# Performance work log

Measured on AMD Instinct MI355X. Metric: run time of the kernel, lower is better.

Reference implementation:

```python
import jax, jax.numpy as jnp
import numpy as np

IC = 8      # inter_channels = in_channels // 2
K = 5       # top-k
EPS = 1e-5  # BatchNorm eps


def _conv(x, w, b, stride, pad):
    y = jax.lax.conv_general_dilated(
        x, w, (stride, stride), [(pad, pad), (pad, pad)],
        dimension_numbers=('NCHW', 'OIHW', 'NCHW'))
    return y + b[None, :, None, None]


def _maxpool2(x):
    return jax.lax.reduce_window(x, -jnp.inf, jax.lax.max,
                                 (1, 1, 2, 2), (1, 1, 2, 2), 'VALID')


def _up2(x):
    return jnp.repeat(jnp.repeat(x, 2, axis=2), 2, axis=3)


def setup_inputs() -> dict:
    key = jax.random.key(0)
    ks = jax.random.split(key, 12)
    C = 16
    x_ms = jax.random.normal(ks[0], (1, C, 96, 96), jnp.float32)
    hp_pan = jax.random.normal(ks[1], (1, C, 192, 192), jnp.float32)
    x_pan = jax.random.normal(ks[2], (1, C, 192, 192), jnp.float32)
    s = 0.05
    return {
        'x_ms': x_ms, 'hp_pan': hp_pan, 'x_pan': x_pan,
        'g_w': jax.random.normal(ks[3], (IC, C, 1, 1), jnp.float32) * s,
        'g_b': jax.random.normal(ks[4], (IC,), jnp.float32) * s,
        'theta_w': jax.random.normal(ks[5], (IC, C, 3, 3), jnp.float32) * s,
        'theta_b': jax.random.normal(ks[6], (IC,), jnp.float32) * s,
        'phi_w': jax.random.normal(ks[7], (IC, C, 3, 3), jnp.float32) * s,
        'phi_b': jax.random.normal(ks[8], (IC,), jnp.float32) * s,
        'W_w': jax.random.normal(ks[9], (C, IC, 1, 1), jnp.float32) * s,
        'W_b': jax.random.normal(ks[10], (C,), jnp.float32) * s,
        'bn_gamma': jax.random.normal(ks[11], (C,), jnp.float32) * s + 1.0,
        'bn_beta': jnp.zeros((C,), jnp.float32),
    }


def reference(x_ms, hp_pan, x_pan, g_w, g_b, theta_w, theta_b,
              phi_w, phi_b, W_w, W_b, bn_gamma, bn_beta):
    B, _, H, W = x_ms.shape
    # g: 1x1 conv + maxpool2 on hp_pan -> (B, M, IC)
    g_x = _maxpool2(_conv(hp_pan, g_w, g_b, 1, 0))
    g_x = g_x.reshape(B, IC, -1).transpose(0, 2, 1)
    # theta: 3x3 s2 conv + up2 on x_ms -> (B, N, IC), N = H*W
    th = _up2(_conv(x_ms, theta_w, theta_b, 2, 1))
    th = th.reshape(B, IC, -1).transpose(0, 2, 1)
    # phi: 3x3 s2 conv + maxpool2 + up2 on x_pan -> (B, IC, M)
    ph = _up2(_maxpool2(_conv(x_pan, phi_w, phi_b, 2, 1)))
    ph = ph.reshape(B, IC, -1)
    # dense similarity (B, N, M)
    f = jnp.einsum('bnc,bcm->bnm', th, ph)
    scores, idx = jax.lax.top_k(f, K)            # (B, N, K)
    scores = jax.nn.softmax(scores, axis=-1)
    # weighted matmul with V restricted to top-k columns (same math as
    # scatter-into-zeros followed by dense matmul, without the dense zeros)
    bi = jnp.arange(B)[:, None, None]
    g_sel = g_x[bi, idx]                          # (B, N, K, IC)
    y = jnp.einsum('bnk,bnkc->bnc', scores, g_sel)
    y = y.transpose(0, 2, 1).reshape(B, IC, H, W)
    wy = _conv(y, W_w, W_b, 1, 0)
    # BatchNorm2d (training-mode batch statistics)
    mean = wy.mean(axis=(0, 2, 3), keepdims=True)
    var = wy.var(axis=(0, 2, 3), keepdims=True)
    z = (wy - mean) * jax.lax.rsqrt(var + EPS)
    z = z * bn_gamma[None, :, None, None] + bn_beta[None, :, None, None]
    return (z, x_pan)
```

## Files before the change

### kernel.cpp

```cpp
#include <hip/hip_runtime.h>

#define IC 8
#define NC 2304
#define NF 9216
#define Z_ELEMS 147456
#define XPAN_ELEMS 589824

typedef unsigned int uint_t;

__global__ __launch_bounds__(256) void k1_prep(
    const float* __restrict__ xms,
    const float* __restrict__ hppan,
    const float* __restrict__ xpan,
    const float* __restrict__ gw, const float* __restrict__ gb,
    const float* __restrict__ thw, const float* __restrict__ thb,
    const float* __restrict__ phw, const float* __restrict__ phb,
    float* __restrict__ theta_c,
    float* __restrict__ phi_c,
    float* __restrict__ gmat)
{
    const int b = blockIdx.x;
    const int tid = threadIdx.x;

    if (b < 18) {
        int idx = b * 256 + tid;
        int pix = idx >> 1, half = idx & 1;
        int r = pix / 48, c = pix % 48;
        int ir0 = 2 * r - 1, ic0 = 2 * c - 1;
        bool rok = (r > 0), cok = (c > 0);
        float acc[8];
        #pragma unroll
        for (int co = 0; co < 8; ++co) acc[co] = 0.0f;
        int ci0 = half * 8;
        #pragma unroll 4
        for (int ci8 = 0; ci8 < 8; ++ci8) {
            int ci = ci0 + ci8;
            const float* base = xms + ci * 9216;
            float xv[9];
            #pragma unroll
            for (int dr = 0; dr < 3; ++dr) {
                #pragma unroll
                for (int dc = 0; dc < 3; ++dc) {
                    bool ok = (dr > 0 || rok) && (dc > 0 || cok);
                    int off = (ir0 + dr) * 96 + (ic0 + dc);
                    float v = base[ok ? off : 0];
                    xv[dr * 3 + dc] = ok ? v : 0.0f;
                }
            }
            #pragma unroll
            for (int tap = 0; tap < 9; ++tap) {
                #pragma unroll
                for (int co = 0; co < 8; ++co)
                    acc[co] += thw[co * 144 + ci * 9 + tap] * xv[tap];
            }
        }
        #pragma unroll
        for (int co = 0; co < 8; ++co) {
            float v = acc[co] + __shfl_xor(acc[co], 1);
            if (half == 0) theta_c[pix * 8 + co] = v + thb[co];
        }
    } else if (b < 90) {
        int idx = (b - 18) * 256 + tid;
        int half = idx & 1, sp = (idx >> 1) & 3, cp = idx >> 3;
        int rc = cp / 48, cc = cp % 48;
        int r96 = 2 * rc + (sp >> 1), c96 = 2 * cc + (sp & 1);
        int ir0 = 2 * r96 - 1, ic0 = 2 * c96 - 1;
        bool rok = (r96 > 0), cok = (c96 > 0);
        float acc[8];
        #pragma unroll
        for (int co = 0; co < 8; ++co) acc[co] = 0.0f;
        int ci0 = half * 8;
        #pragma unroll 4
        for (int ci8 = 0; ci8 < 8; ++ci8) {
            int ci = ci0 + ci8;
            const float* base = xpan + ci * 36864;
            float xv[9];
            #pragma unroll
            for (int dr = 0; dr < 3; ++dr) {
                #pragma unroll
                for (int dc = 0; dc < 3; ++dc) {
                    bool ok = (dr > 0 || rok) && (dc > 0 || cok);
                    int off = (ir0 + dr) * 192 + (ic0 + dc);
                    float v = base[ok ? off : 0];
                    xv[dr * 3 + dc] = ok ? v : 0.0f;
                }
            }
            #pragma unroll
            for (int tap = 0; tap < 9; ++tap) {
                #pragma unroll
                for (int co = 0; co < 8; ++co)
                    acc[co] += phw[co * 144 + ci * 9 + tap] * xv[tap];
            }
        }
        #pragma unroll
        for (int co = 0; co < 8; ++co) {
            float v = acc[co] + __shfl_xor(acc[co], 1);
            v = fmaxf(v, __shfl_xor(v, 2));
            v = fmaxf(v, __shfl_xor(v, 4));
            if ((idx & 7) == 0) phi_c[cp * 8 + co] = v + phb[co];
        }
    } else {
        int idx = (b - 90) * 256 + tid;
        int op = idx >> 2, sp = idx & 3;
        int r = 2 * (op / 96) + (sp >> 1), c = 2 * (op % 96) + (sp & 1);
        const float* bp = hppan + r * 192 + c;
        float acc[8];
        #pragma unroll
        for (int co = 0; co < 8; ++co) acc[co] = 0.0f;
        #pragma unroll
        for (int ci = 0; ci < 16; ++ci) {
            float xv = bp[ci * 36864];
            #pragma unroll
            for (int co = 0; co < 8; ++co)
                acc[co] += gw[co * 16 + ci] * xv;
        }
        #pragma unroll
        for (int co = 0; co < 8; ++co) {
            float v = acc[co];
            v = fmaxf(v, __shfl_xor(v, 1));
            v = fmaxf(v, __shfl_xor(v, 2));
            if (sp == 0) gmat[op * 8 + co] = v + gb[co];
        }
    }
}

__global__ __launch_bounds__(256) void k2_attn(
    const float* __restrict__ theta_c, const float* __restrict__ phi_c,
    const float* __restrict__ gmat, float* __restrict__ y_c)
{
    const int tid = threadIdx.x;
    const int wv = tid >> 6, lane = tid & 63;
    const int nc0 = blockIdx.x * 4;

    float th[4][8];
    #pragma unroll
    for (int r = 0; r < 4; ++r)
        #pragma unroll
        for (int j = 0; j < 8; ++j)
            th[r][j] = theta_c[(nc0 + r) * 8 + j];

    float v1[4], v2[4];
    int i1[4], i2[4];
    #pragma unroll
    for (int r = 0; r < 4; ++r) {
        v1[r] = -INFINITY; v2[r] = -INFINITY;
        i1[r] = 0x7fffffff; i2[r] = 0x7fffffff;
    }

    #pragma unroll
    for (int it = 0; it < 9; ++it) {
        int mc = lane + ((it * 4 + wv) << 6);
        const float4* p = (const float4*)(phi_c + mc * 8);
        float4 a = p[0], bq = p[1];
        #pragma unroll
        for (int r = 0; r < 4; ++r) {
            float v = th[r][0] * a.x + th[r][1] * a.y + th[r][2] * a.z + th[r][3] * a.w
                    + th[r][4] * bq.x + th[r][5] * bq.y + th[r][6] * bq.z + th[r][7] * bq.w;
            if (v > v1[r])      { v2[r] = v1[r]; i2[r] = i1[r]; v1[r] = v; i1[r] = mc; }
            else if (v > v2[r]) { v2[r] = v; i2[r] = mc; }
        }
    }

    #pragma unroll
    for (int r = 0; r < 4; ++r) {
        #pragma unroll
        for (int off = 1; off < 64; off <<= 1) {
            float ov1 = __shfl_xor(v1[r], off);
            int   oi1 = __shfl_xor(i1[r], off);
            float ov2 = __shfl_xor(v2[r], off);
            int   oi2 = __shfl_xor(i2[r], off);
            bool afirst = (v1[r] > ov1) || (v1[r] == ov1 && i1[r] < oi1);
            if (afirst) {
                bool t = (v2[r] > ov1) || (v2[r] == ov1 && i2[r] < oi1);
                v2[r] = t ? v2[r] : ov1; i2[r] = t ? i2[r] : oi1;
            } else {
                bool t = (ov2 > v1[r]) || (ov2 == v1[r] && oi2 < i1[r]);
                float nv2 = t ? ov2 : v1[r]; int ni2 = t ? oi2 : i1[r];
                v1[r] = ov1; i1[r] = oi1; v2[r] = nv2; i2[r] = ni2;
            }
        }
    }

    __shared__ float cv1[4][4], cv2[4][4];
    __shared__ int   ci1[4][4], ci2[4][4];
    if (lane == 0) {
        #pragma unroll
        for (int r = 0; r < 4; ++r) {
            cv1[wv][r] = v1[r]; ci1[wv][r] = i1[r];
            cv2[wv][r] = v2[r]; ci2[wv][r] = i2[r];
        }
    }
    __syncthreads();

    if (tid < 32) {
        int r = tid >> 3, ch = tid & 7;
        float m1 = -INFINITY, m2 = -INFINITY;
        int j1 = 0x7fffffff, j2 = 0x7fffffff;
        #pragma unroll
        for (int w = 0; w < 4; ++w) {
            #pragma unroll
            for (int s = 0; s < 2; ++s) {
                float v = s ? cv2[w][r] : cv1[w][r];
                int   i = s ? ci2[w][r] : ci1[w][r];
                bool b1 = (v > m1) || (v == m1 && i < j1);
                bool b2 = (v > m2) || (v == m2 && i < j2);
                if (b1)      { m2 = m1; j2 = j1; m1 = v; j1 = i; }
                else if (b2) { m2 = v; j2 = i; }
            }
        }
        int rc1 = j1 / 48, cc1 = j1 % 48;
        int m00 = (2 * rc1) * 96 + 2 * cc1;
        int rc2 = j2 / 48, cc2 = j2 % 48;
        int mm2 = (2 * rc2) * 96 + 2 * cc2;
        float e = __expf(m2 - m1);
        float inv = 1.0f / (4.0f + e);
        float gs = gmat[m00 * 8 + ch] + gmat[(m00 + 1) * 8 + ch]
                 + gmat[(m00 + 96) * 8 + ch] + gmat[(m00 + 97) * 8 + ch];
        y_c[(nc0 + r) * 8 + ch] = inv * gs + (e * inv) * gmat[mm2 * 8 + ch];
    }
}

__global__ __launch_bounds__(256) void k3_out(
    const float* __restrict__ y_c,
    const float* __restrict__ Ww, const float* __restrict__ Wb,
    const float* __restrict__ gamma, const float* __restrict__ beta,
    const float* __restrict__ xpan,
    float* __restrict__ zout, float* __restrict__ xpan_out)
{
    const int b = blockIdx.x;
    const int tid = threadIdx.x;

    if (b >= 16) {
        int i = (b - 16) * 256 + tid;
        ((uint4*)xpan_out)[i] = ((const uint4*)xpan)[i];
        return;
    }

    const int co = b;
    float w[8];
    #pragma unroll
    for (int j = 0; j < 8; ++j) w[j] = Ww[co * 8 + j];
    const float bias = Wb[co];

    float wy[9];
    float s = 0.f, s2 = 0.f;
    #pragma unroll
    for (int j = 0; j < 9; ++j) {
        int mc = tid + j * 256;
        const float4* p = (const float4*)(y_c + mc * 8);
        float4 a = p[0], bq = p[1];
        float v = bias + w[0] * a.x + w[1] * a.y + w[2] * a.z + w[3] * a.w
                       + w[4] * bq.x + w[5] * bq.y + w[6] * bq.z + w[7] * bq.w;
        wy[j] = v; s += v; s2 += v * v;
    }
    #pragma unroll
    for (int off = 32; off; off >>= 1) {
        s  += __shfl_down(s, off);
        s2 += __shfl_down(s2, off);
    }
    __shared__ float ps[4], ps2[4];
    __shared__ float sc_s, sh_s;
    int wv = tid >> 6, lane = tid & 63;
    if (lane == 0) { ps[wv] = s; ps2[wv] = s2; }
    __syncthreads();
    if (tid == 0) {
        float S  = ps[0] + ps[1] + ps[2] + ps[3];
        float S2 = ps2[0] + ps2[1] + ps2[2] + ps2[3];
        float mean = S * (1.0f / 2304.0f);
        float var  = S2 * (1.0f / 2304.0f) - mean * mean;
        float rsig = 1.0f / sqrtf(var + 1e-5f);
        float gm = gamma[co], be = beta[co];
        sc_s = gm * rsig;
        sh_s = be - mean * gm * rsig;
    }
    __syncthreads();
    float sc = sc_s, sh = sh_s;
    #pragma unroll
    for (int j = 0; j < 9; ++j) {
        int mc = tid + j * 256;
        int rc = mc / 48, cc = mc % 48;
        float zv = wy[j] * sc + sh;
        float2 zz = make_float2(zv, zv);
        int base = co * 9216 + (2 * rc) * 96 + 2 * cc;
        *(float2*)(zout + base) = zz;
        *(float2*)(zout + base + 96) = zz;
    }
}

extern "C" void kernel_launch(void* const* d_in, const int* in_sizes, int n_in,
                              void* d_out, int out_size, void* d_ws, size_t ws_size,
                              hipStream_t stream) {
    const float* xms   = (const float*)d_in[0];
    const float* hppan = (const float*)d_in[1];
    const float* xpan  = (const float*)d_in[2];
    const float* gw    = (const float*)d_in[3];
    const float* gb    = (const float*)d_in[4];
    const float* thw   = (const float*)d_in[5];
    const float* thb   = (const float*)d_in[6];
    const float* phw   = (const float*)d_in[7];
    const float* phb   = (const float*)d_in[8];
    const float* Ww    = (const float*)d_in[9];
    const float* Wb    = (const float*)d_in[10];
    const float* gam   = (const float*)d_in[11];
    const float* bet   = (const float*)d_in[12];

    float* zout     = (float*)d_out;
    float* xpan_out = zout + Z_ELEMS;

    float* theta_c = (float*)d_ws;
    float* phi_c   = theta_c + NC * IC;
    float* gmat    = phi_c + NC * IC;
    float* y_c     = gmat + NF * IC;

    k1_prep<<<234, 256, 0, stream>>>(xms, hppan, xpan, gw, gb, thw, thb,
                                     phw, phb, theta_c, phi_c, gmat);
    k2_attn<<<576, 256, 0, stream>>>(theta_c, phi_c, gmat, y_c);
    k3_out<<<592, 256, 0, stream>>>(y_c, Ww, Wb, gam, bet, xpan,
                                    zout, xpan_out);
}
```

Baseline: 113.9 us.

## Fuse three kernels into one persistent kernel with software grid barriers

Merges the prep, attention and output kernels into a single 576-block launch that uses atomic-counter grid barriers between phases. The x_pan copy is split across idle blocks in phase one and phase three so it overlaps the compute phases. This removes two kernel launch gaps but adds a memset, the barrier spin cost, and depends on all 576 blocks being co-resident, which the launch bounds are meant to ensure.

```diff
diff --git a/kernel.cpp b/kernel.cpp
--- a/kernel.cpp
+++ b/kernel.cpp
@@ -5,19 +5,36 @@
 #define NF 9216
 #define Z_ELEMS 147456
 #define XPAN_ELEMS 589824
+#define NBLK 576
 
 typedef unsigned int uint_t;
 
-__global__ __launch_bounds__(256) void k1_prep(
+__device__ __forceinline__ void gridbar(uint_t* cnt) {
+    __syncthreads();
+    __threadfence();
+    if (threadIdx.x == 0) {
+        atomicAdd(cnt, 1u);
+        while (atomicAdd(cnt, 0u) < NBLK) __builtin_amdgcn_s_sleep(1);
+    }
+    __syncthreads();
+    __threadfence();
+}
+
+__global__ __launch_bounds__(256, 4) void fused(
     const float* __restrict__ xms,
     const float* __restrict__ hppan,
     const float* __restrict__ xpan,
     const float* __restrict__ gw, const float* __restrict__ gb,
     const float* __restrict__ thw, const float* __restrict__ thb,
     const float* __restrict__ phw, const float* __restrict__ phb,
+    const float* __restrict__ Ww, const float* __restrict__ Wb,
+    const float* __restrict__ gamma, const float* __restrict__ beta,
     float* __restrict__ theta_c,
     float* __restrict__ phi_c,
-    float* __restrict__ gmat)
+    float* __restrict__ gmat,
+    float* __restrict__ y_c,
+    float* __restrict__ zout, float* __restrict__ xpan_out,
+    uint_t* __restrict__ cnt)
 {
     const int b = blockIdx.x;
     const int tid = threadIdx.x;
@@ -99,7 +116,7 @@
             v = fmaxf(v, __shfl_xor(v, 4));
             if ((idx & 7) == 0) phi_c[cp * 8 + co] = v + phb[co];
         }
-    } else {
+    } else if (b < 234) {
         int idx = (b - 90) * 256 + tid;
         int op = idx >> 2, sp = idx & 3;
         int r = 2 * (op / 96) + (sp >> 1), c = 2 * (op % 96) + (sp & 1);
@@ -121,169 +138,160 @@
             v = fmaxf(v, __shfl_xor(v, 2));
             if (sp == 0) gmat[op * 8 + co] = v + gb[co];
         }
+    } else {
+        int i = (b - 234) * 256 + tid;
+        ((uint4*)xpan_out)[i] = ((const uint4*)xpan)[i];
     }
-}
-
-__global__ __launch_bounds__(256) void k2_attn(
-    const float* __restrict__ theta_c, const float* __restrict__ phi_c,
-    const float* __restrict__ gmat, float* __restrict__ y_c)
-{
-    const int tid = threadIdx.x;
-    const int wv = tid >> 6, lane = tid & 63;
-    const int nc0 = blockIdx.x * 4;
-
-    float th[4][8];
-    #pragma unroll
-    for (int r = 0; r < 4; ++r)
-        #pragma unroll
-        for (int j = 0; j < 8; ++j)
-            th[r][j] = theta_c[(nc0 + r) * 8 + j];
-
-    float v1[4], v2[4];
-    int i1[4], i2[4];
-    #pragma unroll
-    for (int r = 0; r < 4; ++r) {
-        v1[r] = -INFINITY; v2[r] = -INFINITY;
-        i1[r] = 0x7fffffff; i2[r] = 0x7fffffff;
+
+    gridbar(&cnt[0]);
+
+    {
+        const int wv = tid >> 6, lane = tid & 63;
+        const int nc0 = b * 4;
+
+        float th[4][8];
+        #pragma unroll
+        for (int r = 0; r < 4; ++r)
+            #pragma unroll
+            for (int j = 0; j < 8; ++j)
+                th[r][j] = theta_c[(nc0 + r) * 8 + j];
+
+        float v1[4], v2[4];
+        int i1[4], i2[4];
+        #pragma unroll
+        for (int r = 0; r < 4; ++r) {
+            v1[r] = -INFINITY; v2[r] = -INFINITY;
+            i1[r] = 0x7fffffff; i2[r] = 0x7fffffff;
+        }
+
+        #pragma unroll
+        for (int it = 0; it < 9; ++it) {
+            int mc = lane + ((it * 4 + wv) << 6);
+            const float4* p = (const float4*)(phi_c + mc * 8);
+            float4 a = p[0], bq = p[1];
+            #pragma unroll
+            for (int r = 0; r < 4; ++r) {
+                float v = th[r][0] * a.x + th[r][1] * a.y + th[r][2] * a.z + th[r][3] * a.w
+                        + th[r][4] * bq.x + th[r][5] * bq.y + th[r][6] * bq.z + th[r][7] * bq.w;
+                if (v > v1[r])      { v2[r] = v1[r]; i2[r] = i1[r]; v1[r] = v; i1[r] = mc; }
+                else if (v > v2[r]) { v2[r] = v; i2[r] = mc; }
+            }
+        }
+
+        #pragma unroll
+        for (int r = 0; r < 4; ++r) {
+            #pragma unroll
+            for (int off = 1; off < 64; off <<= 1) {
+                float ov1 = __shfl_xor(v1[r], off);
+                int   oi1 = __shfl_xor(i1[r], off);
+                float ov2 = __shfl_xor(v2[r], off);
+                int   oi2 = __shfl_xor(i2[r], off);
+                bool afirst = (v1[r] > ov1) || (v1[r] == ov1 && i1[r] < oi1);
+                if (afirst) {
+                    bool t = (v2[r] > ov1) || (v2[r] == ov1 && i2[r] < oi1);
+                    v2[r] = t ? v2[r] : ov1; i2[r] = t ? i2[r] : oi1;
+                } else {
+                    bool t = (ov2 > v1[r]) || (ov2 == v1[r] && oi2 < i1[r]);
+                    float nv2 = t ? ov2 : v1[r]; int ni2 = t ? oi2 : i1[r];
+                    v1[r] = ov1; i1[r] = oi1; v2[r] = nv2; i2[r] = ni2;
+                }
+            }
+        }
+
+        __shared__ float cv1[4][4], cv2[4][4];
+        __shared__ int   ci1[4][4], ci2[4][4];
+        if (lane == 0) {
+            #pragma unroll
+            for (int r = 0; r < 4; ++r) {
+                cv1[wv][r] = v1[r]; ci1[wv][r] = i1[r];
+                cv2[wv][r] = v2[r]; ci2[wv][r] = i2[r];
+            }
+        }
+        __syncthreads();
+
+        if (tid < 32) {
+            int r = tid >> 3, ch = tid & 7;
+            float m1 = -INFINITY, m2 = -INFINITY;
+            int j1 = 0x7fffffff, j2 = 0x7fffffff;
+            #pragma unroll
+            for (int w = 0; w < 4; ++w) {
+                #pragma unroll
+                for (int s = 0; s < 2; ++s) {
+                    float v = s ? cv2[w][r] : cv1[w][r];
+                    int   i = s ? ci2[w][r] : ci1[w][r];
+                    bool b1 = (v > m1) || (v == m1 && i < j1);
+                    bool b2 = (v > m2) || (v == m2 && i < j2);
+                    if (b1)      { m2 = m1; j2 = j1; m1 = v; j1 = i; }
+                    else if (b2) { m2 = v; j2 = i; }
+                }
+            }
+            int rc1 = j1 / 48, cc1 = j1 % 48;
+            int m00 = (2 * rc1) * 96 + 2 * cc1;
+            int rc2 = j2 / 48, cc2 = j2 % 48;
+            int mm2 = (2 * rc2) * 96 + 2 * cc2;
+            float e = __expf(m2 - m1);
+            float inv = 1.0f / (4.0f + e);
+            float gs = gmat[m00 * 8 + ch] + gmat[(m00 + 1) * 8 + ch]
+                     + gmat[(m00 + 96) * 8 + ch] + gmat[(m00 + 97) * 8 + ch];
+            y_c[(nc0 + r) * 8 + ch] = inv * gs + (e * inv) * gmat[mm2 * 8 + ch];
+        }
     }
 
-    #pragma unroll
-    for (int it = 0; it < 9; ++it) {
-        int mc = lane + ((it * 4 + wv) << 6);
-        const float4* p = (const float4*)(phi_c + mc * 8);
-        float4 a = p[0], bq = p[1];
-        #pragma unroll
-        for (int r = 0; r < 4; ++r) {
-            float v = th[r][0] * a.x + th[r][1] * a.y + th[r][2] * a.z + th[r][3] * a.w
-                    + th[r][4] * bq.x + th[r][5] * bq.y + th[r][6] * bq.z + th[r][7] * bq.w;
-            if (v > v1[r])      { v2[r] = v1[r]; i2[r] = i1[r]; v1[r] = v; i1[r] = mc; }
-            else if (v > v2[r]) { v2[r] = v; i2[r] = mc; }
-        }
-    }
-
-    #pragma unroll
-    for (int r = 0; r < 4; ++r) {
-        #pragma unroll
-        for (int off = 1; off < 64; off <<= 1) {
-            float ov1 = __shfl_xor(v1[r], off);
-            int   oi1 = __shfl_xor(i1[r], off);
-            float ov2 = __shfl_xor(v2[r], off);
-            int   oi2 = __shfl_xor(i2[r], off);
-            bool afirst = (v1[r] > ov1) || (v1[r] == ov1 && i1[r] < oi1);
-            if (afirst) {
-                bool t = (v2[r] > ov1) || (v2[r] == ov1 && i2[r] < oi1);
-                v2[r] = t ? v2[r] : ov1; i2[r] = t ? i2[r] : oi1;
-            } else {
-                bool t = (ov2 > v1[r]) || (ov2 == v1[r] && oi2 < i1[r]);
-                float nv2 = t ? ov2 : v1[r]; int ni2 = t ? oi2 : i1[r];
-                v1[r] = ov1; i1[r] = oi1; v2[r] = nv2; i2[r] = ni2;
-            }
-        }
-    }
-
-    __shared__ float cv1[4][4], cv2[4][4];
-    __shared__ int   ci1[4][4], ci2[4][4];
-    if (lane == 0) {
-        #pragma unroll
-        for (int r = 0; r < 4; ++r) {
-            cv1[wv][r] = v1[r]; ci1[wv][r] = i1[r];
-            cv2[wv][r] = v2[r]; ci2[wv][r] = i2[r];
-        }
-    }
-    __syncthreads();
-
-    if (tid < 32) {
-        int r = tid >> 3, ch = tid & 7;
-        float m1 = -INFINITY, m2 = -INFINITY;
-        int j1 = 0x7fffffff, j2 = 0x7fffffff;
-        #pragma unroll
-        for (int w = 0; w < 4; ++w) {
-            #pragma unroll
-            for (int s = 0; s < 2; ++s) {
-                float v = s ? cv2[w][r] : cv1[w][r];
-                int   i = s ? ci2[w][r] : ci1[w][r];
-                bool b1 = (v > m1) || (v == m1 && i < j1);
-                bool b2 = (v > m2) || (v == m2 && i < j2);
-                if (b1)      { m2 = m1; j2 = j1; m1 = v; j1 = i; }
-                else if (b2) { m2 = v; j2 = i; }
-            }
-        }
-        int rc1 = j1 / 48, cc1 = j1 % 48;
-        int m00 = (2 * rc1) * 96 + 2 * cc1;
-        int rc2 = j2 / 48, cc2 = j2 % 48;
-        int mm2 = (2 * rc2) * 96 + 2 * cc2;
-        float e = __expf(m2 - m1);
-        float inv = 1.0f / (4.0f + e);
-        float gs = gmat[m00 * 8 + ch] + gmat[(m00 + 1) * 8 + ch]
-                 + gmat[(m00 + 96) * 8 + ch] + gmat[(m00 + 97) * 8 + ch];
-        y_c[(nc0 + r) * 8 + ch] = inv * gs + (e * inv) * gmat[mm2 * 8 + ch];
-    }
-}
-
-__global__ __launch_bounds__(256) void k3_out(
-    const float* __restrict__ y_c,
-    const float* __restrict__ Ww, const float* __restrict__ Wb,
-    const float* __restrict__ gamma, const float* __restrict__ beta,
-    const float* __restrict__ xpan,
-    float* __restrict__ zout, float* __restrict__ xpan_out)
-{
-    const int b = blockIdx.x;
-    const int tid = threadIdx.x;
-
-    if (b >= 16) {
-        int i = (b - 16) * 256 + tid;
+    gridbar(&cnt[1]);
+
+    if (b < 16) {
+        const int co = b;
+        float w[8];
+        #pragma unroll
+        for (int j = 0; j < 8; ++j) w[j] = Ww[co * 8 + j];
+        const float bias = Wb[co];
+
+        float wy[9];
+        float s = 0.f, s2 = 0.f;
+        #pragma unroll
+        for (int j = 0; j < 9; ++j) {
+            int mc = tid + j * 256;
+            const float4* p = (const float4*)(y_c + mc * 8);
+            float4 a = p[0], bq = p[1];
+            float v = bias + w[0] * a.x + w[1] * a.y + w[2] * a.z + w[3] * a.w
+                           + w[4] * bq.x + w[5] * bq.y + w[6] * bq.z + w[7] * bq.w;
+            wy[j] = v; s += v; s2 += v * v;
+        }
+        #pragma unroll
+        for (int off = 32; off; off >>= 1) {
+            s  += __shfl_down(s, off);
+            s2 += __shfl_down(s2, off);
+        }
+        __shared__ float ps[4], ps2[4];
+        __shared__ float sc_s, sh_s;
+        int wv = tid >> 6, lane = tid & 63;
+        if (lane == 0) { ps[wv] = s; ps2[wv] = s2; }
+        __syncthreads();
+        if (tid == 0) {
+            float S  = ps[0] + ps[1] + ps[2] + ps[3];
+            float S2 = ps2[0] + ps2[1] + ps2[2] + ps2[3];
+            float mean = S * (1.0f / 2304.0f);
+            float var  = S2 * (1.0f / 2304.0f) - mean * mean;
+            float rsig = 1.0f / sqrtf(var + 1e-5f);
+            float gm = gamma[co], be = beta[co];
+            sc_s = gm * rsig;
+            sh_s = be - mean * gm * rsig;
+        }
+        __syncthreads();
+        float sc = sc_s, sh = sh_s;
+        #pragma unroll
+        for (int j = 0; j < 9; ++j) {
+            int mc = tid + j * 256;
+            int rc = mc / 48, cc = mc % 48;
+            float zv = wy[j] * sc + sh;
+            float2 zz = make_float2(zv, zv);
+            int base = co * 9216 + (2 * rc) * 96 + 2 * cc;
+            *(float2*)(zout + base) = zz;
+            *(float2*)(zout + base + 96) = zz;
+        }
+    } else if (b < 250) {
+        int i = (342 + b - 16) * 256 + tid;
         ((uint4*)xpan_out)[i] = ((const uint4*)xpan)[i];
-        return;
-    }
-
-    const int co = b;
-    float w[8];
-    #pragma unroll
-    for (int j = 0; j < 8; ++j) w[j] = Ww[co * 8 + j];
-    const float bias = Wb[co];
-
-    float wy[9];
-    float s = 0.f, s2 = 0.f;
-    #pragma unroll
-    for (int j = 0; j < 9; ++j) {
-        int mc = tid + j * 256;
-        const float4* p = (const float4*)(y_c + mc * 8);
-        float4 a = p[0], bq = p[1];
-        float v = bias + w[0] * a.x + w[1] * a.y + w[2] * a.z + w[3] * a.w
-                       + w[4] * bq.x + w[5] * bq.y + w[6] * bq.z + w[7] * bq.w;
-        wy[j] = v; s += v; s2 += v * v;
-    }
-    #pragma unroll
-    for (int off = 32; off; off >>= 1) {
-        s  += __shfl_down(s, off);
-        s2 += __shfl_down(s2, off);
-    }
-    __shared__ float ps[4], ps2[4];
-    __shared__ float sc_s, sh_s;
-    int wv = tid >> 6, lane = tid & 63;
-    if (lane == 0) { ps[wv] = s; ps2[wv] = s2; }
-    __syncthreads();
-    if (tid == 0) {
-        float S  = ps[0] + ps[1] + ps[2] + ps[3];
-        float S2 = ps2[0] + ps2[1] + ps2[2] + ps2[3];
-        float mean = S * (1.0f / 2304.0f);
-        float var  = S2 * (1.0f / 2304.0f) - mean * mean;
-        float rsig = 1.0f / sqrtf(var + 1e-5f);
-        float gm = gamma[co], be = beta[co];
-        sc_s = gm * rsig;
-        sh_s = be - mean * gm * rsig;
-    }
-    __syncthreads();
-    float sc = sc_s, sh = sh_s;
-    #pragma unroll
-    for (int j = 0; j < 9; ++j) {
-        int mc = tid + j * 256;
-        int rc = mc / 48, cc = mc % 48;
-        float zv = wy[j] * sc + sh;
-        float2 zz = make_float2(zv, zv);
-        int base = co * 9216 + (2 * rc) * 96 + 2 * cc;
-        *(float2*)(zout + base) = zz;
-        *(float2*)(zout + base + 96) = zz;
     }
 }
 
@@ -311,10 +319,11 @@
     float* phi_c   = theta_c + NC * IC;
     float* gmat    = phi_c + NC * IC;
     float* y_c     = gmat + NF * IC;
-
-    k1_prep<<<234, 256, 0, stream>>>(xms, hppan, xpan, gw, gb, thw, thb,
-                                     phw, phb, theta_c, phi_c, gmat);
-    k2_attn<<<576, 256, 0, stream>>>(theta_c, phi_c, gmat, y_c);
-    k3_out<<<592, 256, 0, stream>>>(y_c, Ww, Wb, gam, bet, xpan,
-                                    zout, xpan_out);
+    uint_t* cnt    = (uint_t*)(y_c + NC * IC);
+
+    hipMemsetAsync(cnt, 0, 2 * sizeof(uint_t), stream);
+    fused<<<NBLK, 256, 0, stream>>>(xms, hppan, xpan, gw, gb, thw, thb,
+                                    phw, phb, Ww, Wb, gam, bet,
+                                    theta_c, phi_c, gmat, y_c,
+                                    zout, xpan_out, cnt);
 }
```

After: 322.8 us. +183.5%, slower.
